# Optimization experiments

Hardware: AMD Instinct MI355X
Metric: run time of the kernel (lower is better)

## Reference

```python
import jax, jax.numpy as jnp
import numpy as np

H = 512  # hidden_num

def _lstm_cell(x, h, c, Wih, Whh, bih, bhh):
    # PyTorch LSTMCell: gates ordered i, f, g, o
    gates = x @ Wih.T + bih + h @ Whh.T + bhh  # [B, 4H]
    i, f, g, o = jnp.split(gates, 4, axis=-1)
    i = jax.nn.sigmoid(i)
    f = jax.nn.sigmoid(f)
    g = jnp.tanh(g)
    o = jax.nn.sigmoid(o)
    c_new = f * c + i * g
    h_new = o * jnp.tanh(c_new)
    return h_new, c_new


def setup_inputs() -> dict:
    key = jax.random.key(0)
    ks = jax.random.split(key, 12)
    B, T = 256, 1024
    s1 = 1.0 / np.sqrt(H)
    u = lambda k, shape: jax.random.uniform(k, shape, jnp.float32, -s1, s1)
    return {
        "input": jax.random.normal(ks[0], (B, T), dtype=jnp.float32),
        "pred_len": 64,
        "Wih1": u(ks[1], (4 * H, 1)),
        "Whh1": u(ks[2], (4 * H, H)),
        "bih1": u(ks[3], (4 * H,)),
        "bhh1": u(ks[4], (4 * H,)),
        "Wih2": u(ks[5], (4 * H, H)),
        "Whh2": u(ks[6], (4 * H, H)),
        "bih2": u(ks[7], (4 * H,)),
        "bhh2": u(ks[8], (4 * H,)),
        "Wlin": u(ks[9], (1, H)),
        "blin": u(ks[10], (1,)),
    }


def reference(input, pred_len, Wih1, Whh1, bih1, bhh1, Wih2, Whh2, bih2, bhh2, Wlin, blin):
    B = input.shape[0]
    z = jnp.zeros((B, H), dtype=input.dtype)
    xs = input.T[:, :, None]  # [T, B, 1]

    def step(carry, x_t):
        h1, c1, h2, c2 = carry
        h1, c1 = _lstm_cell(x_t, h1, c1, Wih1, Whh1, bih1, bhh1)
        h2, c2 = _lstm_cell(h1, h2, c2, Wih2, Whh2, bih2, bhh2)
        return (h1, c1, h2, c2), None

    (h1, c1, h2, c2), _ = jax.lax.scan(step, (z, z, z, z), xs)
    out = h2 @ Wlin.T + blin  # [B, 1]
    first = out[-1, :]        # [1]

    def ar_step(carry, _):
        h1, c1, h2, c2, o = carry
        h1, c1 = _lstm_cell(o, h1, c1, Wih1, Whh1, bih1, bhh1)
        h2, c2 = _lstm_cell(h1, h2, c2, Wih2, Whh2, bih2, bhh2)
        o = h2 @ Wlin.T + blin
        return (h1, c1, h2, c2, o), o[-1, :]

    if pred_len - 1 > 0:
        _, ys = jax.lax.scan(ar_step, (h1, c1, h2, c2, out), None, length=pred_len - 1)
        return jnp.concatenate([first, ys.reshape(-1)])  # [pred_len]
    return first
```

## Files before the change

kernel.cpp:

```cpp
#include <hip/hip_runtime.h>
#include <math.h>


#define G     64
#define NT    512
#define HD    512
#define TT    1024
#define PRED  64
#define LINEF 64
#define SLOTF (G*LINEF)
#define STR   264
#define AS    __HIP_MEMORY_SCOPE_AGENT

typedef unsigned long long u64;

#define LOG2E  1.44269504088896340736f

#define KEEP4(v) asm volatile("" : "+v"(v.x), "+v"(v.y), "+v"(v.z), "+v"(v.w))

__device__ __forceinline__ float sigf(float x){
  return __builtin_amdgcn_rcpf(1.0f + __builtin_amdgcn_exp2f(-LOG2E * x));
}
__device__ __forceinline__ float tanhf_fast(float x){
  float e = __builtin_amdgcn_exp2f(2.0f * LOG2E * x);
  return 1.0f - 2.0f * __builtin_amdgcn_rcpf(e + 1.0f);
}
__device__ __forceinline__ float dot4(float4 a, float4 b){
  return a.x*b.x + a.y*b.y + a.z*b.z + a.w*b.w;
}

__global__ __launch_bounds__(NT, 1) void lstm2_kernel(
    const float* __restrict__ input,
    const float* __restrict__ Wih1, const float* __restrict__ Whh1,
    const float* __restrict__ bih1, const float* __restrict__ bhh1,
    const float* __restrict__ Wih2, const float* __restrict__ Whh2,
    const float* __restrict__ bih2, const float* __restrict__ bhh2,
    const float* __restrict__ Wlin, const float* __restrict__ blin,
    float* __restrict__ out, float* __restrict__ ws)
{
  __shared__ __align__(16) float hvec[4*STR];
  __shared__ __align__(16) float xrow[TT];
  __shared__ float pre[64];

  float* comm = ws;

  const int t  = threadIdx.x;
  const int wg = blockIdx.x;
  const int rg = t >> 6;
  const int sg = t & 63;

  ((float2*)xrow)[t] = ((const float2*)(input + 255*TT))[t];

  float4 w1[4][2], w2[4][4];
  #pragma unroll
  for (int k=0;k<4;k++){
    const int r = rg*4 + k;
    const int R = (r>>3)*HD + wg*8 + (r&7);
    const float* pa = Whh1 + R*HD + sg*8;
    w1[k][0] = *(const float4*)(pa);
    w1[k][1] = *(const float4*)(pa+4);
    const float* pb = Wih2 + R*HD + sg*8;
    const float* pc = Whh2 + R*HD + sg*8;
    w2[k][0] = *(const float4*)(pb);
    w2[k][1] = *(const float4*)(pb+4);
    w2[k][2] = *(const float4*)(pc);
    w2[k][3] = *(const float4*)(pc+4);
  }
  #pragma unroll
  for (int k=0;k<4;k++){
    KEEP4(w1[k][0]); KEEP4(w1[k][1]);
    KEEP4(w2[k][0]); KEEP4(w2[k][1]); KEEP4(w2[k][2]); KEEP4(w2[k][3]);
  }

  float bias[4]={0,0,0,0}, wx[4]={0,0,0,0};
  float cst  = 0.f;
  float hcur = 0.f;
  if (t < 8){
    #pragma unroll
    for (int q=0;q<4;q++){
      int R = q*HD + wg*8 + t;
      bias[q] = bih1[R] + bhh1[R];
      wx[q]   = Wih1[R];
    }
  } else if (t < 16){
    #pragma unroll
    for (int q=0;q<4;q++){
      int R = q*HD + wg*8 + (t-8);
      bias[q] = bih2[R] + bhh2[R];
    }
  }
  float4 wl0={0,0,0,0}, wl1={0,0,0,0};
  if (t < 64){
    wl0 = *(const float4*)(Wlin + t*8);
    wl1 = *(const float4*)(Wlin + t*8 + 4);
  }
  const float blin0 = blin[0];

  auto poll_stage = [&](unsigned g){
    const int w = t >> 3, j = t & 7;
    const u64* dq = (const u64*)(comm + (g & 1u)*SLOTF + w*LINEF) + 2*j;
    u64 q0, q1;
    do {
      q0 = __hip_atomic_load(dq,     __ATOMIC_RELAXED, AS);
      q1 = __hip_atomic_load(dq + 1, __ATOMIC_RELAXED, AS);
    } while ((unsigned)(q0 >> 32) != g || (unsigned)(q1 >> 32) != g);
    const int c  = j >> 1;
    const int wd = c*STR + 4*w + 2*(j & 1);
    float2 fv;
    fv.x = __builtin_bit_cast(float, (unsigned)q0);
    fv.y = __builtin_bit_cast(float, (unsigned)q1);
    *(float2*)(hvec + wd) = fv;
    __syncthreads();
  };

  auto dots_reduce = [&](){
    const float4 c0 = ((const float4*)(hvec + 0*STR))[sg];
    const float4 c1 = ((const float4*)(hvec + 1*STR))[sg];
    const float4 c2 = ((const float4*)(hvec + 2*STR))[sg];
    const float4 c3 = ((const float4*)(hvec + 3*STR))[sg];
    float v[8];
    #pragma unroll
    for (int k=0;k<4;k++){
      v[k]   = dot4(w1[k][0],c0) + dot4(w1[k][1],c1);
      v[4+k] = dot4(w2[k][0],c0) + dot4(w2[k][1],c1)
             + dot4(w2[k][2],c2) + dot4(w2[k][3],c3);
    }
    const int b0 = sg & 1, b1 = (sg>>1)&1, b2 = (sg>>2)&1;
    float k4[4];
    #pragma unroll
    for (int k=0;k<4;k++){
      float x = b0 ? v[k] : v[k+4];
      float y = __shfl_xor(x, 1, 64);
      k4[k] = (b0 ? v[k+4] : v[k]) + y;
    }
    float k2[2];
    #pragma unroll
    for (int k=0;k<2;k++){
      float x = b1 ? k4[k] : k4[k+2];
      float y = __shfl_xor(x, 2, 64);
      k2[k] = (b1 ? k4[k+2] : k4[k]) + y;
    }
    float k1;
    {
      float x = b2 ? k2[0] : k2[1];
      float y = __shfl_xor(x, 4, 64);
      k1 = (b2 ? k2[1] : k2[0]) + y;
    }
    k1 += __shfl_xor(k1, 8, 64);
    k1 += __shfl_xor(k1, 16, 64);
    k1 += __shfl_xor(k1, 32, 64);
    if (sg < 8){
      const int j = b0*4 + b1*2 + b2;
      if (j < 4) pre[rg*4 + j]        = k1;
      else       pre[32 + rg*4 + j-4] = k1;
    }
  };

  auto tail = [&](unsigned g, bool d1, bool d2, float xv){
    if (rg == 0){
      const float rsum = pre[t];
      const int u  = t & 7;
      const int s0 = (t < 8) ? t : (32 + u);
      float pi = __shfl(rsum, s0,      64);
      float pf = __shfl(rsum, s0 + 8,  64);
      float pg = __shfl(rsum, s0 + 16, 64);
      float po = __shfl(rsum, s0 + 24, 64);
      const bool act = (t < 8) ? d1 : ((t < 16) ? d2 : false);
      if (act){
        if (t < 8){
          pi += xv*wx[0] + bias[0];
          pf += xv*wx[1] + bias[1];
          pg += xv*wx[2] + bias[2];
          po += xv*wx[3] + bias[3];
        } else {
          pi += bias[0]; pf += bias[1]; pg += bias[2]; po += bias[3];
        }
        cst  = sigf(pf)*cst + sigf(pi)*tanhf_fast(pg);
        hcur = sigf(po)*tanhf_fast(cst);
      }
      if (t < 16){
        u64 pr = ((u64)(g + 1u) << 32) | (u64)__builtin_bit_cast(unsigned, hcur);
        u64* nb = (u64*)(comm + ((g+1u) & 1u)*SLOTF + wg*LINEF);
        __hip_atomic_store(nb + t, pr, __ATOMIC_RELAXED, AS);
      }
    }
  };

  auto computeO = [&](int oi, float& xv){
    if (rg == 0){
      float s = dot4(wl0, ((const float4*)(hvec + 2*STR))[t])
              + dot4(wl1, ((const float4*)(hvec + 3*STR))[t]);
      #pragma unroll
      for (int m=1;m<64;m<<=1) s += __shfl_xor(s, m, 64);
      xv = s + blin0;
      if (wg == 0 && t == 0) out[oi] = xv;
    }
  };

  __syncthreads();

  unsigned g = 0;

  for (int tk=0; tk<TT; ++tk, ++g){
    poll_stage(g);
    dots_reduce();
    __syncthreads();
    tail(g, true, tk >= 1, xrow[tk]);
  }

  poll_stage(g);
  dots_reduce();
  __syncthreads();
  tail(g, false, true, 0.f);
  ++g;

  for (int s=TT; s<TT+PRED-1; ++s){
    poll_stage(g);
    float xv = 0.f;
    computeO(s - TT, xv);
    dots_reduce();
    __syncthreads();
    tail(g, true, false, xv);
    ++g;

    poll_stage(g);
    dots_reduce();
    __syncthreads();
    tail(g, false, true, 0.f);
    ++g;
  }

  poll_stage(g);
  float xv;
  computeO(PRED - 1, xv);
}

extern "C" void kernel_launch(void* const* d_in, const int* in_sizes, int n_in,
                              void* d_out, int out_size, void* d_ws, size_t ws_size,
                              hipStream_t stream) {
  const float* input = (const float*)d_in[0];
  const float* Wih1 = (const float*)d_in[2];
  const float* Whh1 = (const float*)d_in[3];
  const float* bih1 = (const float*)d_in[4];
  const float* bhh1 = (const float*)d_in[5];
  const float* Wih2 = (const float*)d_in[6];
  const float* Whh2 = (const float*)d_in[7];
  const float* bih2 = (const float*)d_in[8];
  const float* bhh2 = (const float*)d_in[9];
  const float* Wlin = (const float*)d_in[10];
  const float* blin = (const float*)d_in[11];

  hipMemsetAsync(d_ws, 0, 2 * SLOTF * sizeof(float), stream);

  lstm2_kernel<<<dim3(G), dim3(NT), 0, stream>>>(
      input, Wih1, Whh1, bih1, bhh1, Wih2, Whh2, bih2, bhh2, Wlin, blin,
      (float*)d_out, (float*)d_ws);
}
```

Before: 2.065 ms.

## Assign one hidden unit per wave and drop second block barrier per step

Each wave now owns one hidden unit for both layers, holding all four gate rows of that unit. The full gate reduction and cell update stay inside the wave through shuffles, so the shared `pre` buffer and the second __syncthreads per step are gone. The shared h vector is double-buffered by step parity so the next step's poll writes cannot race with reads of the current step. Every wave now runs the activation math redundantly, and the output projection is computed in every wave, which adds some ALU work and shuffles per step.

```diff
diff --git a/kernel.cpp b/kernel.cpp
--- a/kernel.cpp
+++ b/kernel.cpp
@@ -38,9 +38,8 @@
     const float* __restrict__ Wlin, const float* __restrict__ blin,
     float* __restrict__ out, float* __restrict__ ws)
 {
-  __shared__ __align__(16) float hvec[4*STR];
+  __shared__ __align__(16) float hvec[2][4*STR];
   __shared__ __align__(16) float xrow[TT];
-  __shared__ float pre[64];
 
   float* comm = ws;
 
@@ -48,82 +47,79 @@
   const int wg = blockIdx.x;
   const int rg = t >> 6;
   const int sg = t & 63;
+  const int U  = wg*8 + rg;
 
   ((float2*)xrow)[t] = ((const float2*)(input + 255*TT))[t];
 
-  float4 w1[4][2], w2[4][4];
+  float4 w1[4][2], w2x[4][2], w2h[4][2];
   #pragma unroll
-  for (int k=0;k<4;k++){
-    const int r = rg*4 + k;
-    const int R = (r>>3)*HD + wg*8 + (r&7);
+  for (int q=0;q<4;q++){
+    const int R = q*HD + U;
     const float* pa = Whh1 + R*HD + sg*8;
-    w1[k][0] = *(const float4*)(pa);
-    w1[k][1] = *(const float4*)(pa+4);
+    w1[q][0]  = *(const float4*)(pa);
+    w1[q][1]  = *(const float4*)(pa+4);
     const float* pb = Wih2 + R*HD + sg*8;
+    w2x[q][0] = *(const float4*)(pb);
+    w2x[q][1] = *(const float4*)(pb+4);
     const float* pc = Whh2 + R*HD + sg*8;
-    w2[k][0] = *(const float4*)(pb);
-    w2[k][1] = *(const float4*)(pb+4);
-    w2[k][2] = *(const float4*)(pc);
-    w2[k][3] = *(const float4*)(pc+4);
+    w2h[q][0] = *(const float4*)(pc);
+    w2h[q][1] = *(const float4*)(pc+4);
   }
   #pragma unroll
-  for (int k=0;k<4;k++){
-    KEEP4(w1[k][0]); KEEP4(w1[k][1]);
-    KEEP4(w2[k][0]); KEEP4(w2[k][1]); KEEP4(w2[k][2]); KEEP4(w2[k][3]);
+  for (int q=0;q<4;q++){
+    KEEP4(w1[q][0]);  KEEP4(w1[q][1]);
+    KEEP4(w2x[q][0]); KEEP4(w2x[q][1]);
+    KEEP4(w2h[q][0]); KEEP4(w2h[q][1]);
   }
 
   float bias[4]={0,0,0,0}, wx[4]={0,0,0,0};
+  if (sg < 2){
+    const float* bi = sg ? bih2 : bih1;
+    const float* bh = sg ? bhh2 : bhh1;
+    #pragma unroll
+    for (int q=0;q<4;q++){
+      const int R = q*HD + U;
+      bias[q] = bi[R] + bh[R];
+      if (sg == 0) wx[q] = Wih1[R];
+    }
+  }
+  float4 wl0 = *(const float4*)(Wlin + sg*8);
+  float4 wl1 = *(const float4*)(Wlin + sg*8 + 4);
+  const float blin0 = blin[0];
+
   float cst  = 0.f;
   float hcur = 0.f;
-  if (t < 8){
-    #pragma unroll
-    for (int q=0;q<4;q++){
-      int R = q*HD + wg*8 + t;
-      bias[q] = bih1[R] + bhh1[R];
-      wx[q]   = Wih1[R];
-    }
-  } else if (t < 16){
-    #pragma unroll
-    for (int q=0;q<4;q++){
-      int R = q*HD + wg*8 + (t-8);
-      bias[q] = bih2[R] + bhh2[R];
-    }
-  }
-  float4 wl0={0,0,0,0}, wl1={0,0,0,0};
-  if (t < 64){
-    wl0 = *(const float4*)(Wlin + t*8);
-    wl1 = *(const float4*)(Wlin + t*8 + 4);
-  }
-  const float blin0 = blin[0];
 
   auto poll_stage = [&](unsigned g){
     const int w = t >> 3, j = t & 7;
     const u64* dq = (const u64*)(comm + (g & 1u)*SLOTF + w*LINEF) + 2*j;
-    u64 q0, q1;
-    do {
+    u64 q0 = __hip_atomic_load(dq,     __ATOMIC_RELAXED, AS);
+    u64 q1 = __hip_atomic_load(dq + 1, __ATOMIC_RELAXED, AS);
+    while ((unsigned)(q0 >> 32) != g || (unsigned)(q1 >> 32) != g){
       q0 = __hip_atomic_load(dq,     __ATOMIC_RELAXED, AS);
       q1 = __hip_atomic_load(dq + 1, __ATOMIC_RELAXED, AS);
-    } while ((unsigned)(q0 >> 32) != g || (unsigned)(q1 >> 32) != g);
+    }
     const int c  = j >> 1;
     const int wd = c*STR + 4*w + 2*(j & 1);
     float2 fv;
     fv.x = __builtin_bit_cast(float, (unsigned)q0);
     fv.y = __builtin_bit_cast(float, (unsigned)q1);
-    *(float2*)(hvec + wd) = fv;
+    *(float2*)(hvec[g & 1u] + wd) = fv;
     __syncthreads();
   };
 
-  auto dots_reduce = [&](){
-    const float4 c0 = ((const float4*)(hvec + 0*STR))[sg];
-    const float4 c1 = ((const float4*)(hvec + 1*STR))[sg];
-    const float4 c2 = ((const float4*)(hvec + 2*STR))[sg];
-    const float4 c3 = ((const float4*)(hvec + 3*STR))[sg];
+  auto tick = [&](unsigned g, bool d1, bool d2, float xv){
+    const float* hv = hvec[g & 1u];
+    const float4 c0 = ((const float4*)(hv + 0*STR))[sg];
+    const float4 c1 = ((const float4*)(hv + 1*STR))[sg];
+    const float4 c2 = ((const float4*)(hv + 2*STR))[sg];
+    const float4 c3 = ((const float4*)(hv + 3*STR))[sg];
     float v[8];
     #pragma unroll
     for (int k=0;k<4;k++){
       v[k]   = dot4(w1[k][0],c0) + dot4(w1[k][1],c1);
-      v[4+k] = dot4(w2[k][0],c0) + dot4(w2[k][1],c1)
-             + dot4(w2[k][2],c2) + dot4(w2[k][3],c3);
+      v[4+k] = dot4(w2x[k][0],c0) + dot4(w2x[k][1],c1)
+             + dot4(w2h[k][0],c2) + dot4(w2h[k][1],c3);
     }
     const int b0 = sg & 1, b1 = (sg>>1)&1, b2 = (sg>>2)&1;
     float k4[4];
@@ -149,52 +145,34 @@
     k1 += __shfl_xor(k1, 8, 64);
     k1 += __shfl_xor(k1, 16, 64);
     k1 += __shfl_xor(k1, 32, 64);
-    if (sg < 8){
-      const int j = b0*4 + b1*2 + b2;
-      if (j < 4) pre[rg*4 + j]        = k1;
-      else       pre[32 + rg*4 + j-4] = k1;
+    const int p = sg & 1;
+    float pi = __shfl(k1, p,     64);
+    float pf = __shfl(k1, 4 + p, 64);
+    float pg = __shfl(k1, 2 + p, 64);
+    float po = __shfl(k1, 6 + p, 64);
+    const float xb = p ? 0.f : xv;
+    pi += xb*wx[0] + bias[0];
+    pf += xb*wx[1] + bias[1];
+    pg += xb*wx[2] + bias[2];
+    po += xb*wx[3] + bias[3];
+    const bool act = p ? d2 : d1;
+    float cn = sigf(pf)*cst + sigf(pi)*tanhf_fast(pg);
+    float hn = sigf(po)*tanhf_fast(cn);
+    if (act){ cst = cn; hcur = hn; }
+    if (sg < 2){
+      u64 pr = ((u64)(g + 1u) << 32) | (u64)__builtin_bit_cast(unsigned, hcur);
+      u64* nb = (u64*)(comm + ((g+1u) & 1u)*SLOTF + wg*LINEF);
+      __hip_atomic_store(nb + rg + 8*sg, pr, __ATOMIC_RELAXED, AS);
     }
   };
 
-  auto tail = [&](unsigned g, bool d1, bool d2, float xv){
-    if (rg == 0){
-      const float rsum = pre[t];
-      const int u  = t & 7;
-      const int s0 = (t < 8) ? t : (32 + u);
-      float pi = __shfl(rsum, s0,      64);
-      float pf = __shfl(rsum, s0 + 8,  64);
-      float pg = __shfl(rsum, s0 + 16, 64);
-      float po = __shfl(rsum, s0 + 24, 64);
-      const bool act = (t < 8) ? d1 : ((t < 16) ? d2 : false);
-      if (act){
-        if (t < 8){
-          pi += xv*wx[0] + bias[0];
-          pf += xv*wx[1] + bias[1];
-          pg += xv*wx[2] + bias[2];
-          po += xv*wx[3] + bias[3];
-        } else {
-          pi += bias[0]; pf += bias[1]; pg += bias[2]; po += bias[3];
-        }
-        cst  = sigf(pf)*cst + sigf(pi)*tanhf_fast(pg);
-        hcur = sigf(po)*tanhf_fast(cst);
-      }
-      if (t < 16){
-        u64 pr = ((u64)(g + 1u) << 32) | (u64)__builtin_bit_cast(unsigned, hcur);
-        u64* nb = (u64*)(comm + ((g+1u) & 1u)*SLOTF + wg*LINEF);
-        __hip_atomic_store(nb + t, pr, __ATOMIC_RELAXED, AS);
-      }
-    }
-  };
-
-  auto computeO = [&](int oi, float& xv){
-    if (rg == 0){
-      float s = dot4(wl0, ((const float4*)(hvec + 2*STR))[t])
-              + dot4(wl1, ((const float4*)(hvec + 3*STR))[t]);
-      #pragma unroll
-      for (int m=1;m<64;m<<=1) s += __shfl_xor(s, m, 64);
-      xv = s + blin0;
-      if (wg == 0 && t == 0) out[oi] = xv;
-    }
+  auto computeO = [&](unsigned g)->float{
+    const float* hv = hvec[g & 1u];
+    float s = dot4(wl0, ((const float4*)(hv + 2*STR))[sg])
+            + dot4(wl1, ((const float4*)(hv + 3*STR))[sg]);
+    #pragma unroll
+    for (int m=1;m<64;m<<=1) s += __shfl_xor(s, m, 64);
+    return s + blin0;
   };
 
   __syncthreads();
@@ -203,36 +181,28 @@
 
   for (int tk=0; tk<TT; ++tk, ++g){
     poll_stage(g);
-    dots_reduce();
-    __syncthreads();
-    tail(g, true, tk >= 1, xrow[tk]);
+    tick(g, true, tk >= 1, xrow[tk]);
   }
 
   poll_stage(g);
-  dots_reduce();
-  __syncthreads();
-  tail(g, false, true, 0.f);
+  tick(g, false, true, 0.f);
   ++g;
 
   for (int s=TT; s<TT+PRED-1; ++s){
     poll_stage(g);
-    float xv = 0.f;
-    computeO(s - TT, xv);
-    dots_reduce();
-    __syncthreads();
-    tail(g, true, false, xv);
+    float xv = computeO(g);
+    if (wg == 0 && t == 0) out[s - TT] = xv;
+    tick(g, true, false, xv);
     ++g;
 
     poll_stage(g);
-    dots_reduce();
-    __syncthreads();
-    tail(g, false, true, 0.f);
+    tick(g, false, true, 0.f);
     ++g;
   }
 
   poll_stage(g);
-  float xv;
-  computeO(PRED - 1, xv);
+  float xv = computeO(g);
+  if (wg == 0 && t == 0) out[PRED - 1] = xv;
 }
 
 extern "C" void kernel_launch(void* const* d_in, const int* in_sizes, int n_in,
```

Measured after the change: 3.639 ms. +76.3%, slower.
